# Kernel optimization log

Hardware: AMD Instinct MI355X
Metric: run time of the kernel (lower is better)

Reference implementation:

```python
import jax, jax.numpy as jnp
import numpy as np

H = 2048          # hidden_size
HK = 16           # linear_num_key_heads
HV = 32           # linear_num_value_heads
DK = 128          # linear_key_head_dim
DV = 128          # linear_value_head_dim
KW = 4            # linear_conv_kernel_dim
KEY_DIM = HK * DK   # 2048
VAL_DIM = HV * DV   # 4096
CONV_DIM = 2 * KEY_DIM + VAL_DIM  # 8192
T = 4096
EPS = 1e-6


def setup_inputs() -> dict:
    key = jax.random.key(0)
    ks = jax.random.split(key, 8)
    w = lambda k, shape, sc=0.02: (jax.random.normal(k, shape, jnp.float32) * sc)
    return {
        "hidden_states": jax.random.normal(ks[0], (T, H), jnp.float32),
        "W_qkvz": w(ks[1], (H, 2 * KEY_DIM + 2 * VAL_DIM)),   # q,k,v,z merged proj
        "W_ba": w(ks[2], (H, 2 * HV)),                        # b,a merged proj
        "conv_w": w(ks[3], (CONV_DIM, KW), 0.1),              # depthwise causal conv
        "A_log": jnp.log(jax.random.uniform(ks[4], (HV,), jnp.float32, 1.0, 16.0)),
        "dt_bias": jnp.ones((HV,), jnp.float32),
        "norm_w": jnp.ones((DV,), jnp.float32),
        "W_out": w(ks[5], (VAL_DIM, H)),
    }


def _l2norm(x):
    return x * jax.lax.rsqrt(jnp.sum(x * x, axis=-1, keepdims=True) + 1e-6)


def reference(hidden_states, W_qkvz, W_ba, conv_w, A_log, dt_bias, norm_w, W_out):
    T_ = hidden_states.shape[0]
    # 1. merged input projections
    qkvz = hidden_states @ W_qkvz                     # [T, 2*key+2*val]
    ba = hidden_states @ W_ba                         # [T, 2*HV]
    q, k, v, z = jnp.split(qkvz, [KEY_DIM, 2 * KEY_DIM, 2 * KEY_DIM + VAL_DIM], axis=-1)
    b, a = jnp.split(ba, 2, axis=-1)

    # 2. short causal depthwise conv1d over q|k|v (z is NOT convolved), then SiLU
    qkv = jnp.concatenate([q, k, v], axis=-1)         # [T, CONV_DIM]
    xp = jnp.pad(qkv, ((KW - 1, 0), (0, 0)))
    y = sum(xp[j:j + T_] * conv_w[:, j] for j in range(KW))
    qkv = jax.nn.silu(y)
    q, k, v = jnp.split(qkv, [KEY_DIM, 2 * KEY_DIM], axis=-1)

    q = _l2norm(q.reshape(T_, HK, DK)) * (DK ** -0.5)
    k = _l2norm(k.reshape(T_, HK, DK))
    v = v.reshape(T_, HV, DV)
    z = z.reshape(T_, HV, DV)

    # GQA-style head expansion
    r = HV // HK
    q = jnp.repeat(q, r, axis=1)                      # [T, HV, DK]
    k = jnp.repeat(k, r, axis=1)

    # gating / delta coefficients
    g = -jnp.exp(A_log) * jax.nn.softplus(a + dt_bias)  # [T, HV] log-decay
    beta = jax.nn.sigmoid(b)                            # [T, HV]

    # 3. gated delta rule recurrence: S_t = exp(g_t)*S + beta_t*k_t(v_t - k_t^T exp(g_t) S)
    def step(S, inp):
        q_t, k_t, v_t, g_t, b_t = inp
        S = S * jnp.exp(g_t)[:, None, None]             # [HV, DK, DV]
        kv = jnp.einsum('hd,hdv->hv', k_t, S)
        delta = (v_t - kv) * b_t[:, None]
        S = S + jnp.einsum('hd,hv->hdv', k_t, delta)
        o_t = jnp.einsum('hd,hdv->hv', q_t, S)
        return S, o_t

    S0 = jnp.zeros((HV, DK, DV), jnp.float32)
    _, o = jax.lax.scan(step, S0, (q, k, v, g, beta))   # o: [T, HV, DV]

    # 4. gated RMSNorm (norm_before_gate=True): rmsnorm(o)*w, then * silu(z)
    var = jnp.mean(o * o, axis=-1, keepdims=True)
    o = o * jax.lax.rsqrt(var + EPS) * norm_w
    o = o * jax.nn.silu(z)

    # 5. output projection
    return o.reshape(T_, VAL_DIM) @ W_out
```

## Files before the change

### kernel.cpp

```cpp
#include <hip/hip_runtime.h>
#include <hip/hip_bf16.h>

#define T_LEN 4096
#define H_DIM 2048
#define HKn 16
#define HVn 32
#define DKn 128
#define DVn 128
#define KEY_DIM 2048
#define VAL_DIM 4096

typedef unsigned int u32;
typedef unsigned short u16;
typedef __attribute__((ext_vector_type(8))) short bf16x8;
typedef __attribute__((ext_vector_type(4))) float f32x4;

__device__ __forceinline__ u16 f2bf(float x){
  u32 u = __float_as_uint(x);
  u32 r = (u + 0x7fffu + ((u>>16)&1u)) >> 16;
  return (u16)r;
}
__device__ __forceinline__ float bf2f(u32 b){ return __uint_as_float(b<<16); }
__device__ __forceinline__ u32 packbf(float a, float b){ return (u32)f2bf(a) | ((u32)f2bf(b)<<16); }

__global__ __launch_bounds__(256) void k_cvt(const float* __restrict__ in, u16* __restrict__ out, int n){
  int i = (blockIdx.x*256 + threadIdx.x)*8;
  if (i >= n) return;
  float4 a = *(const float4*)(in+i);
  float4 b = *(const float4*)(in+i+4);
  uint4 o;
  o.x = packbf(a.x,a.y); o.y = packbf(a.z,a.w);
  o.z = packbf(b.x,b.y); o.w = packbf(b.z,b.w);
  *(uint4*)(out+i) = o;
}

__global__ __launch_bounds__(256) void k_tcvt(const float* __restrict__ in, u16* __restrict__ out, int R, int C){
  __shared__ float tile[32][33];
  int c0 = blockIdx.x*32, r0 = blockIdx.y*32;
  int tx = threadIdx.x & 31, ty = threadIdx.x >> 5;
#pragma unroll
  for (int i=0;i<4;++i) tile[ty+8*i][tx] = in[(size_t)(r0+ty+8*i)*C + c0+tx];
  __syncthreads();
#pragma unroll
  for (int i=0;i<4;++i) out[(size_t)(c0+ty+8*i)*R + r0+tx] = f2bf(tile[tx][ty+8*i]);
}

__global__ __launch_bounds__(256) void k_ba(const float* __restrict__ X, const float* __restrict__ W,
    const float* __restrict__ A_log, const float* __restrict__ dt_bias,
    float* __restrict__ gT, float* __restrict__ bT){
  int tid = threadIdx.x;
  int t = blockIdx.x*4 + (tid>>6);
  int j = tid & 63;
  const float* xr = X + (size_t)t*H_DIM;
  float acc = 0.f;
  for (int k=0;k<H_DIM;k+=4){
    float4 xv = *(const float4*)(xr+k);
    acc += xv.x*W[(size_t)(k+0)*64 + j];
    acc += xv.y*W[(size_t)(k+1)*64 + j];
    acc += xv.z*W[(size_t)(k+2)*64 + j];
    acc += xv.w*W[(size_t)(k+3)*64 + j];
  }
  if (j < HVn) {
    bT[(size_t)j*T_LEN + t] = 1.f/(1.f+__expf(-acc));
  } else {
    int h = j - HVn;
    float x = acc + dt_bias[h];
    float sp = (x > 20.f) ? x : log1pf(__expf(x));
    gT[(size_t)h*T_LEN + t] = -__expf(A_log[h]) * sp;
  }
}

typedef const __attribute__((address_space(1))) u32* gas_t;
typedef __attribute__((address_space(3))) u32* las_t;
__device__ __forceinline__ void gld16(const void* g, void* l){
  __builtin_amdgcn_global_load_lds((gas_t)g, (las_t)l, 16, 0, 0);
}
__device__ __forceinline__ f32x4 mf(bf16x8 a, bf16x8 b, f32x4 c){
  return __builtin_amdgcn_mfma_f32_16x16x32_bf16(a,b,c,0,0,0);
}

#define G2_LDS 131072
#define SWX(a) ((a) ^ ((((a)>>9)&1)<<5))

template<int WRITE_BF16>
__global__ __launch_bounds__(512) void k_g256(const u16* __restrict__ A, const u16* __restrict__ BT,
    void* __restrict__ C1, void* __restrict__ C2, int NS, int M, int N, int K){
  extern __shared__ char sm[];
  const int tid=threadIdx.x, lane=tid&63, wave=tid>>6;
  const int fr=lane&15, fq=lane>>4;
  const int wm=wave>>2, wn=wave&3;
  const int nbm = M>>8, nwg = nbm*(N>>8);
  const int cpx = nwg>>3;
  const int swz = ((int)blockIdx.x & 7)*cpx + ((int)blockIdx.x >> 3);
  const int m0 = (swz % nbm) << 8, n0 = (swz / nbm) << 8;
  const int NK = K >> 5;

  f32x4 acc[8][4];
#pragma unroll
  for (int i=0;i<8;++i)
#pragma unroll
    for (int j=0;j<4;++j) acc[i][j] = (f32x4){0.f,0.f,0.f,0.f};

  auto stageA=[&](int kt){
    char* base = sm + (size_t)(kt&3)*32768;
#pragma unroll
    for (int ld=0; ld<2; ++ld){
      int p = ld*8192 + wave*1024 + lane*16;
      int a = SWX(p);
      gld16((const char*)A + ((size_t)(m0 + (a>>6))*K + kt*32)*2 + (a&63), base + p);
    }
  };
  auto stageB=[&](int kt){
    char* base = sm + (size_t)(kt&3)*32768 + 16384;
#pragma unroll
    for (int ld=0; ld<2; ++ld){
      int p = ld*8192 + wave*1024 + lane*16;
      int a = SWX(p);
      gld16((const char*)BT + ((size_t)(n0 + (a>>6))*K + kt*32)*2 + (a&63), base + p);
    }
  };

  stageA(0); stageB(0); stageA(1); stageB(1); stageA(2); stageB(2);
  __syncthreads();

  bf16x8 bcur[4], bnxt[4], a0f[4], a1f[4];
  {
    const char* bufA = sm;
    const char* bufB = sm + 16384;
#pragma unroll
    for (int j=0;j<4;++j){
      int a = (wn*64 + j*16 + fr)*64 + fq*16;
      bcur[j] = *(const bf16x8*)(bufB + SWX(a));
    }
#pragma unroll
    for (int i=0;i<4;++i){
      int a = (wm*128 + i*16 + fr)*64 + fq*16;
      a0f[i] = *(const bf16x8*)(bufA + SWX(a));
    }
  }

  for (int kt=0; kt<NK; ++kt){
    const char* bufA = sm + (size_t)(kt&3)*32768;
    if (kt+3 < NK) stageA(kt+3);
#pragma unroll
    for (int i=0;i<4;++i){
      int a = (wm*128 + 64 + i*16 + fr)*64 + fq*16;
      a1f[i] = *(const bf16x8*)(bufA + SWX(a));
    }
    asm volatile("s_waitcnt vmcnt(6)" ::: "memory");
    asm volatile("s_barrier" ::: "memory");
    __builtin_amdgcn_s_setprio(1);
#pragma unroll
    for (int i=0;i<4;++i)
#pragma unroll
      for (int j=0;j<4;++j) acc[i][j] = mf(a0f[i], bcur[j], acc[i][j]);
    __builtin_amdgcn_s_setprio(0);
    asm volatile("s_barrier" ::: "memory");
    if (kt+3 < NK) stageB(kt+3);
    if (kt+1 < NK){
      const char* nA = sm + (size_t)((kt+1)&3)*32768;
      const char* nB = nA + 16384;
#pragma unroll
      for (int j=0;j<4;++j){
        int a = (wn*64 + j*16 + fr)*64 + fq*16;
        bnxt[j] = *(const bf16x8*)(nB + SWX(a));
      }
#pragma unroll
      for (int i=0;i<4;++i){
        int a = (wm*128 + i*16 + fr)*64 + fq*16;
        a0f[i] = *(const bf16x8*)(nA + SWX(a));
      }
    }
    asm volatile("s_barrier" ::: "memory");
    __builtin_amdgcn_s_setprio(1);
#pragma unroll
    for (int i=0;i<4;++i)
#pragma unroll
      for (int j=0;j<4;++j) acc[4+i][j] = mf(a1f[i], bcur[j], acc[4+i][j]);
    __builtin_amdgcn_s_setprio(0);
    asm volatile("s_barrier" ::: "memory");
#pragma unroll
    for (int j=0;j<4;++j) bcur[j] = bnxt[j];
  }

#pragma unroll
  for (int mt=0; mt<8; ++mt)
#pragma unroll
    for (int nt=0; nt<4; ++nt){
      int row = m0 + wm*128 + mt*16 + fq*4;
      int col = n0 + wn*64 + nt*16 + fr;
#pragma unroll
      for (int r=0;r<4;++r){
        float v = acc[mt][nt][r];
        if (col < NS){
          if (WRITE_BF16) ((u16*)C1)[(size_t)(row+r)*NS + col] = f2bf(v);
          else            ((float*)C1)[(size_t)(row+r)*NS + col] = v;
        } else {
          if (WRITE_BF16) ((u16*)C2)[(size_t)(row+r)*(N-NS) + col-NS] = f2bf(v);
          else            ((float*)C2)[(size_t)(row+r)*(N-NS) + col-NS] = v;
        }
      }
    }
}

__global__ __launch_bounds__(256) void k_conv(const u16* __restrict__ qkv, const float* __restrict__ cw,
    u16* __restrict__ qn, u16* __restrict__ kn, u16* __restrict__ vv){
  int t = blockIdx.x;
  int region = blockIdx.y;
  int c = region*2048 + threadIdx.x*8;
  float wgt[8][4];
#pragma unroll
  for (int i=0;i<8;++i){
    float4 wv = *(const float4*)(cw + (size_t)(c+i)*4);
    wgt[i][0]=wv.x; wgt[i][1]=wv.y; wgt[i][2]=wv.z; wgt[i][3]=wv.w;
  }
  float y[8];
#pragma unroll
  for (int i=0;i<8;++i) y[i]=0.f;
#pragma unroll
  for (int j=0;j<4;++j){
    int tt = t + j - 3;
    if (tt < 0) continue;
    uint4 raw = *(const uint4*)(qkv + (size_t)tt*8192 + c);
    float xv[8];
    xv[0]=bf2f(raw.x&0xffffu); xv[1]=bf2f(raw.x>>16);
    xv[2]=bf2f(raw.y&0xffffu); xv[3]=bf2f(raw.y>>16);
    xv[4]=bf2f(raw.z&0xffffu); xv[5]=bf2f(raw.z>>16);
    xv[6]=bf2f(raw.w&0xffffu); xv[7]=bf2f(raw.w>>16);
#pragma unroll
    for (int i=0;i<8;++i) y[i] += xv[i]*wgt[i][j];
  }
#pragma unroll
  for (int i=0;i<8;++i){ y[i] = y[i] / (1.f + __expf(-y[i])); }

  if (region <= 1){
    float ss = 0.f;
#pragma unroll
    for (int i=0;i<8;++i) ss += y[i]*y[i];
    ss += __shfl_xor(ss,1); ss += __shfl_xor(ss,2);
    ss += __shfl_xor(ss,4); ss += __shfl_xor(ss,8);
    float sc = 1.f/sqrtf(ss + 1e-6f);
    if (region==0) sc *= 0.08838834764831845f;
#pragma unroll
    for (int i=0;i<8;++i) y[i]*=sc;
    u16* dst = (region==0 ? qn : kn) + (size_t)t*KEY_DIM + (c - region*2048);
    *(uint4*)dst = make_uint4(packbf(y[0],y[1]),packbf(y[2],y[3]),packbf(y[4],y[5]),packbf(y[6],y[7]));
  } else {
    u16* dst = vv + (size_t)t*VAL_DIM + (c - 4096);
    *(uint4*)dst = make_uint4(packbf(y[0],y[1]),packbf(y[2],y[3]),packbf(y[4],y[5]),packbf(y[6],y[7]));
  }
}

#define P1_K    0
#define P1_Q    16384
#define P1_KT   32768
#define P1_NBP  49152
#define P1_AQ   57344
#define P1_DT   65536
#define P1_WMT  73728
#define P1_NBD  81920
#define P1_TII  86016
#define P1_R1T  90112
#define P1_TAB  94208
#define P1_SIZE 95296

#define SW7(r,cb) ((cb) ^ (((r)&7)<<4))
#define SW3(r,cb) ((cb) ^ (((r)&3)<<4))
#define aK(r,cb)   (P1_K   + (r)*256 + SW7(r,cb))
#define aQ2(r,cb)  (P1_Q   + (r)*256 + SW7(r,cb))
#define aKT(d,cb)  (P1_KT  + (d)*128 + SW7(d,cb))
#define aNBP(t,cb) (P1_NBP + (t)*128 + SW7(t,cb))
#define aAQ(t,cb)  (P1_AQ  + (t)*128 + SW7(t,cb))
#define aDT(s,cb)  (P1_DT  + (s)*128 + SW7(s,cb))
#define aWMT(s,cb) (P1_WMT + (s)*128 + SW7(s,cb))
#define aTII(b,r,cb) (P1_TII + (b)*1024 + (r)*64 + SW3(r,cb))
#define aR1T(v,cb)   (P1_R1T + (v)*64 + SW3(v,cb))

__global__ __launch_bounds__(256) void k_prep(const u16* __restrict__ qn, const u16* __restrict__ kn,
    const float* __restrict__ gT, const float* __restrict__ bT,
    u16* __restrict__ aqmg, u16* __restrict__ kwmg, float* __restrict__ tabg){
  extern __shared__ char sm[];
  const int tid=threadIdx.x, lane=tid&63, wave=tid>>6;
  const int fr=lane&15, fq=lane>>4;
  const int b=blockIdx.x, h=b>>6, c=b&63, kh=h>>1;
  const f32x4 z4={0.f,0.f,0.f,0.f};
  for (int off=P1_DT+tid*16; off<P1_TAB; off+=4096) *(uint4*)(sm+off)=make_uint4(0,0,0,0);
  {
    int srow = wave*4 + (lane>>4);
    int pb = (lane&15)*16;
#pragma unroll
    for (int r=0;r<4;++r){
      int row=r*16+srow;
      int gcb = pb ^ ((row&7)<<4);
      gld16((const char*)kn + ((size_t)((c<<6)+row)*KEY_DIM + kh*DKn)*2 + gcb, sm + P1_K + r*4096 + wave*1024);
      gld16((const char*)qn + ((size_t)((c<<6)+row)*KEY_DIM + kh*DKn)*2 + gcb, sm + P1_Q + r*4096 + wave*1024);
    }
  }
  float* TB=(float*)(sm+P1_TAB);
  if (wave==0){
    int t=lane;
    float gv=gT[(size_t)h*T_LEN+(c<<6)+t];
    float bv=bT[(size_t)h*T_LEN+(c<<6)+t];
    float s=gv;
    for(int o2=1;o2<64;o2<<=1){ float u=__shfl_up(s,o2,64); if(lane>=o2) s+=u; }
    float cgL=__shfl(s,63,64);
    float gam=__expf(s);
    TB[t]=s; TB[64+t]=gam; TB[128+t]=__expf(cgL-s); TB[192+t]=bv;
    float* tg=tabg+(size_t)b*192;
    tg[t]=gam; tg[64+t]=bv;
    if(t==0) tg[128]=__expf(cgL);
  }
  __syncthreads();
#pragma unroll
  for (int dd=0;dd<2;++dd){
    int tp=tid&31, d0=((tid>>5)+dd*8)*8;
    bf16x8 r0=*(const bf16x8*)(sm+aK(2*tp,d0*2));
    bf16x8 r1=*(const bf16x8*)(sm+aK(2*tp+1,d0*2));
#pragma unroll
    for(int j=0;j<8;++j){
      u32 pk=((u32)(u16)r0[j])|((u32)(u16)r1[j]<<16);
      *(u32*)(sm+aKT(d0+j,tp*4))=pk;
    }
  }
  const int ra=(wave>>1)*32, rb=(wave&1)*32;
  f32x4 kq[2][2], qk[2][2];
#pragma unroll
  for(int ta=0;ta<2;++ta)
#pragma unroll
  for(int tb=0;tb<2;++tb){ kq[ta][tb]=z4; qk[ta][tb]=z4; }
#pragma unroll
  for(int kk=0;kk<4;++kk){
    int cb=kk*64+fq*16;
    bf16x8 Ak0=*(const bf16x8*)(sm+aK(ra+fr,cb));
    bf16x8 Ak1=*(const bf16x8*)(sm+aK(ra+16+fr,cb));
    bf16x8 Aq0=*(const bf16x8*)(sm+aQ2(ra+fr,cb));
    bf16x8 Aq1=*(const bf16x8*)(sm+aQ2(ra+16+fr,cb));
    bf16x8 Bk0=*(const bf16x8*)(sm+aK(rb+fr,cb));
    bf16x8 Bk1=*(const bf16x8*)(sm+aK(rb+16+fr,cb));
    if(ra>=rb)      { kq[0][0]=mf(Ak0,Bk0,kq[0][0]); qk[0][0]=mf(Aq0,Bk0,qk[0][0]); }
    if(ra>=rb+16)   { kq[0][1]=mf(Ak0,Bk1,kq[0][1]); qk[0][1]=mf(Aq0,Bk1,qk[0][1]); }
    if(ra+16>=rb)   { kq[1][0]=mf(Ak1,Bk0,kq[1][0]); qk[1][0]=mf(Aq1,Bk0,qk[1][0]); }
    if(ra+16>=rb+16){ kq[1][1]=mf(Ak1,Bk1,kq[1][1]); qk[1][1]=mf(Aq1,Bk1,qk[1][1]); }
  }
  {
    const float* cg=TB; const float* Be=TB+192;
#pragma unroll
    for(int ta=0;ta<2;++ta)
#pragma unroll
    for(int tb=0;tb<2;++tb){
      int tab=ra+16*ta, tbb=rb+16*tb;
#pragma unroll
      for(int p=0;p<4;++p){
        int t=tab+fq*4+p, s2=tbb+fr;
        float e=__expf(cg[t]-cg[s2]);
        float nv=(s2<t)? -Be[t]*kq[ta][tb][p]*e : 0.f;
        *(u16*)(sm+aNBP(t,s2*2)) = (tbb<tab)? f2bf(nv):(u16)0;
        if(tbb==tab) ((float*)(sm+P1_NBD))[(tab>>4)*256+(fq*4+p)*16+fr]=nv;
        float av=(s2<=t)? qk[ta][tb][p]*e : 0.f;
        *(u16*)(sm+aAQ(t,s2*2)) = f2bf(av);
      }
    }
  }
  __syncthreads();
  {
    int r=lane&15;
    const float* nb=(const float*)(sm+P1_NBD)+wave*256+r*16;
    float n[16], t_[16];
#pragma unroll
    for(int j=0;j<16;++j){ n[j]=nb[j]; t_[j]=(j==r)?1.f:0.f; }
#pragma unroll
    for(int s=0;s<15;++s){
      float tsj[16];
#pragma unroll
      for(int j=0;j<16;++j)
        tsj[j]=__int_as_float(__builtin_amdgcn_ds_bpermute(s*4,__float_as_int(t_[j])));
      if(r>s){
#pragma unroll
        for(int j=0;j<16;++j) t_[j]=fmaf(n[s],tsj[j],t_[j]);
      }
    }
    if(lane<16){
      u32 pk[8];
#pragma unroll
      for(int j=0;j<8;++j) pk[j]=packbf(t_[2*j],t_[2*j+1]);
      *(uint4*)(sm+aTII(wave,r,0)) =make_uint4(pk[0],pk[1],pk[2],pk[3]);
      *(uint4*)(sm+aTII(wave,r,16))=make_uint4(pk[4],pk[5],pk[6],pk[7]);
    }
  }
  __syncthreads();
  {
    const float* WV=TB+128;
    int vb=16*wave;
    for(int i=0;i<4;++i){
      f32x4 acc;
#pragma unroll
      for(int p=0;p<4;++p) acc[p]=(vb+fr==16*i+fq*4+p)?1.f:0.f;
      int np=(i+1)>>1;
      for(int jp=0;jp<np;++jp){
        bf16x8 A=*(const bf16x8*)(sm+aNBP(16*i+fr,jp*64+fq*16));
        bf16x8 B=*(const bf16x8*)(sm+aDT(vb+fr,jp*64+fq*16));
        acc=mf(A,B,acc);
      }
      uint2 w1; w1.x=packbf(acc[0],acc[1]); w1.y=packbf(acc[2],acc[3]);
      *(uint2*)(sm+aR1T(vb+fr,fq*8))=w1;
      bf16x8 At=*(const bf16x8*)(sm+aTII(i,fr,fq*16));
      bf16x8 Bt=*(const bf16x8*)(sm+aR1T(vb+fr,fq*16));
      f32x4 dl=mf(At,Bt,z4);
      int s0=16*i+fq*4;
      uint2 wd; wd.x=packbf(dl[0],dl[1]); wd.y=packbf(dl[2],dl[3]);
      *(uint2*)(sm+aDT(vb+fr,s0*2))=wd;
      uint2 ww; ww.x=packbf(dl[0]*WV[s0],dl[1]*WV[s0+1]); ww.y=packbf(dl[2]*WV[s0+2],dl[3]*WV[s0+3]);
      *(uint2*)(sm+aWMT(vb+fr,s0*2))=ww;
    }
  }
  __syncthreads();
  {
    u16* aout = aqmg + (size_t)b*4096;
#pragma unroll
    for(int ts=0;ts<4;++ts){
      f32x4 acc=z4;
#pragma unroll
      for(int jp=0;jp<2;++jp){
        bf16x8 A=*(const bf16x8*)(sm+aAQ(16*wave+fr,jp*64+fq*16));
        bf16x8 B=*(const bf16x8*)(sm+aDT(16*ts+fr,jp*64+fq*16));
        acc=mf(A,B,acc);
      }
#pragma unroll
      for(int p=0;p<4;++p){
        int t=16*wave+fq*4+p, s=16*ts+fr;
        aout[(t*128 + ((s*2)^((t&7)<<4)))>>1]=f2bf(acc[p]);
      }
    }
    u16* kout = kwmg + (size_t)b*8192;
#pragma unroll
    for(int j=0;j<2;++j){
      int dt=wave+4*j;
#pragma unroll
      for(int st=0;st<4;++st){
        f32x4 acc=z4;
#pragma unroll
        for(int jp=0;jp<2;++jp){
          bf16x8 A=*(const bf16x8*)(sm+aKT(16*dt+fr,jp*64+fq*16));
          bf16x8 B=*(const bf16x8*)(sm+aWMT(16*st+fr,jp*64+fq*16));
          acc=mf(A,B,acc);
        }
#pragma unroll
        for(int p=0;p<4;++p){
          int d=16*dt+fq*4+p, s=16*st+fr;
          kout[(d*128 + ((s*2)^((d&7)<<4)))>>1]=f2bf(acc[p]);
        }
      }
    }
  }
}

#define P2_K(b)   ((b)*16384)
#define P2_Q(b)   (32768 + (b)*16384)
#define P2_W(b)   (65536 + (b)*16384)
#define P2_M(b)   (98304 + (b)*8192)
#define P2_TAB(b) (114688 + (b)*1024)
#define P2_ST(b)  (116736 + (b)*4096)
#define P2_R0T    124928
#define P2_SIZE   126976

#define bKx(b,r,cb)  (P2_K(b) + (r)*256 + SW7(r,cb))
#define bQx(b,r,cb)  (P2_Q(b) + (r)*256 + SW7(r,cb))
#define bWx(b,d,cb)  (P2_W(b) + (d)*128 + SW7(d,cb))
#define bMx(b,t,cb)  (P2_M(b) + (t)*128 + SW7(t,cb))
#define bSTx(b,v,cb) (P2_ST(b) + (v)*256 + SW7(v,cb))
#define bRx(v,cb)    (P2_R0T + (v)*128 + SW7(v,cb))

__global__ __launch_bounds__(256) void k_state(const u16* __restrict__ qn, const u16* __restrict__ kn,
    const u16* __restrict__ vv, const u16* __restrict__ aqmg, const u16* __restrict__ kwmg,
    const float* __restrict__ tabg, float* __restrict__ o){
  extern __shared__ char sm[];
  const int tid=threadIdx.x, lane=tid&63, wave=tid>>6;
  const int fr=lane&15, fq=lane>>4;
  const int h=blockIdx.x&31, vs=(blockIdx.x>>5)*16, kh=h>>1;
  const f32x4 z4={0.f,0.f,0.f,0.f};
  for(int off=116736+tid*16; off<124928; off+=4096) *(uint4*)(sm+off)=make_uint4(0,0,0,0);

  auto stage=[&](int c,int b){
    int srow=wave*4+(lane>>4);
    int pb2=(lane&15)*16;
#pragma unroll
    for(int r=0;r<4;++r){
      int row=r*16+srow;
      int gcb=pb2^((row&7)<<4);
      gld16((const char*)kn + ((size_t)((c<<6)+row)*KEY_DIM + kh*DKn)*2 + gcb, sm + P2_K(b)+r*4096+wave*1024);
      gld16((const char*)qn + ((size_t)((c<<6)+row)*KEY_DIM + kh*DKn)*2 + gcb, sm + P2_Q(b)+r*4096+wave*1024);
    }
    const char* wsrc=(const char*)kwmg + (size_t)(h*64+c)*16384;
#pragma unroll
    for(int r=0;r<4;++r)
      gld16(wsrc + r*4096 + wave*1024 + lane*16, sm + P2_W(b)+r*4096+wave*1024);
    const char* msrc=(const char*)aqmg + (size_t)(h*64+c)*8192;
#pragma unroll
    for(int r=0;r<2;++r)
      gld16(msrc + r*4096 + wave*1024 + lane*16, sm + P2_M(b)+r*4096+wave*1024);
    if(wave==0)
      gld16((const char*)tabg + (size_t)(h*64+c)*768 + lane*16, sm + P2_TAB(b));
  };
  u16 vl[4];
  auto loadV=[&](int c){
#pragma unroll
    for(int p=0;p<4;++p)
      vl[p]=vv[(size_t)((c<<6)+16*wave+fq*4+p)*VAL_DIM + h*DVn + vs + fr];
  };

  f32x4 S0=z4, S1=z4;
  stage(0,0); loadV(0);
  __syncthreads();

  for(int c=0;c<64;++c){
    int b=c&1;
    const float* TBf=(const float*)(sm+P2_TAB(b));
    f32x4 ks=z4;
#pragma unroll
    for(int kk=0;kk<4;++kk)
      ks=mf(*(const bf16x8*)(sm+bKx(b,16*wave+fr,kk*64+fq*16)),
            *(const bf16x8*)(sm+bSTx(b,fr,kk*64+fq*16)), ks);
    float r0v[4];
#pragma unroll
    for(int p=0;p<4;++p){
      int t=16*wave+fq*4+p;
      r0v[p]=TBf[64+t]*(bf2f(vl[p]) - TBf[t]*ks[p]);
    }
    uint2 rw; rw.x=packbf(r0v[0],r0v[1]); rw.y=packbf(r0v[2],r0v[3]);
    *(uint2*)(sm+bRx(fr,32*wave+8*fq))=rw;
    __syncthreads();
    if(c<63) stage(c+1,b^1);
    f32x4 qs=z4;
#pragma unroll
    for(int kk=0;kk<4;++kk)
      qs=mf(*(const bf16x8*)(sm+bQx(b,16*wave+fr,kk*64+fq*16)),
            *(const bf16x8*)(sm+bSTx(b,fr,kk*64+fq*16)), qs);
#pragma unroll
    for(int p=0;p<4;++p) qs[p]*=TBf[16*wave+fq*4+p];
#pragma unroll
    for(int jp=0;jp<2;++jp)
      qs=mf(*(const bf16x8*)(sm+bMx(b,16*wave+fr,jp*64+fq*16)),
            *(const bf16x8*)(sm+bRx(fr,jp*64+fq*16)), qs);
#pragma unroll
    for(int p=0;p<4;++p)
      o[(size_t)((c<<6)+16*wave+fq*4+p)*VAL_DIM + h*DVn + vs + fr]=qs[p];
    if(c<63) loadV(c+1);
    float gl=TBf[128];
    S0[0]*=gl;S0[1]*=gl;S0[2]*=gl;S0[3]*=gl;
    S1[0]*=gl;S1[1]*=gl;S1[2]*=gl;S1[3]*=gl;
#pragma unroll
    for(int jp=0;jp<2;++jp){
      bf16x8 Br=*(const bf16x8*)(sm+bRx(fr,jp*64+fq*16));
      S0=mf(*(const bf16x8*)(sm+bWx(b,16*wave+fr,jp*64+fq*16)), Br, S0);
      S1=mf(*(const bf16x8*)(sm+bWx(b,16*(wave+4)+fr,jp*64+fq*16)), Br, S1);
    }
    uint2 s0w; s0w.x=packbf(S0[0],S0[1]); s0w.y=packbf(S0[2],S0[3]);
    *(uint2*)(sm+bSTx(b^1,fr,32*wave+8*fq))=s0w;
    uint2 s1w; s1w.x=packbf(S1[0],S1[1]); s1w.y=packbf(S1[2],S1[3]);
    *(uint2*)(sm+bSTx(b^1,fr,32*(wave+4)+8*fq))=s1w;
    __syncthreads();
  }
}

__global__ __launch_bounds__(256) void k_gnorm(const float* __restrict__ o, const u16* __restrict__ zq,
    const float* __restrict__ nw, u16* __restrict__ og){
  int t = blockIdx.x;
  int base = threadIdx.x*16;
  const float* src = o + (size_t)t*VAL_DIM + base;
  float x[16];
#pragma unroll
  for (int i=0;i<4;++i){
    float4 f = *(const float4*)(src + i*4);
    x[i*4+0]=f.x; x[i*4+1]=f.y; x[i*4+2]=f.z; x[i*4+3]=f.w;
  }
  float ss=0.f;
#pragma unroll
  for (int i=0;i<16;++i) ss += x[i]*x[i];
  ss += __shfl_xor(ss,1); ss += __shfl_xor(ss,2); ss += __shfl_xor(ss,4);
  float rs = 1.f/sqrtf(ss*(1.f/128.f) + 1e-6f);
  const u16* zp = zq + (size_t)t*VAL_DIM + base;
  uint4 z0 = *(const uint4*)zp;
  uint4 z1 = *(const uint4*)(zp+8);
  u32 zr[8] = {z0.x,z0.y,z0.z,z0.w,z1.x,z1.y,z1.z,z1.w};
  u32 outw[8];
#pragma unroll
  for (int p=0;p<8;++p){
    float za = bf2f(zr[p]&0xffffu), zb = bf2f(zr[p]>>16);
    float sa = za/(1.f+__expf(-za)), sb = zb/(1.f+__expf(-zb));
    int i0 = p*2, i1 = p*2+1;
    float oa = x[i0]*rs*nw[(base+i0)&127]*sa;
    float ob = x[i1]*rs*nw[(base+i1)&127]*sb;
    outw[p] = packbf(oa, ob);
  }
  uint4* dst = (uint4*)(og + (size_t)t*VAL_DIM + base);
  dst[0] = make_uint4(outw[0],outw[1],outw[2],outw[3]);
  dst[1] = make_uint4(outw[4],outw[5],outw[6],outw[7]);
}

extern "C" void kernel_launch(void* const* d_in, const int* in_sizes, int n_in,
                              void* d_out, int out_size, void* d_ws, size_t ws_size,
                              hipStream_t stream) {
  const float* hidden  = (const float*)d_in[0];
  const float* W_qkvz  = (const float*)d_in[1];
  const float* W_ba    = (const float*)d_in[2];
  const float* conv_w  = (const float*)d_in[3];
  const float* A_log   = (const float*)d_in[4];
  const float* dt_bias = (const float*)d_in[5];
  const float* norm_w  = (const float*)d_in[6];
  const float* W_out   = (const float*)d_in[7];

  char* w = (char*)d_ws;
  size_t need = 252706816;
  if (ws_size < need) return;

  u16*   Xb   = (u16*)(w + 0);
  u16*   W1T  = (u16*)(w + 16777216);
  u16*   QKV  = (u16*)(w + 67108864);
  u16*   Z    = (u16*)(w + 134217728);
  u16*   QN   = (u16*)(w + 167772160);
  u16*   KN   = (u16*)(w + 184549376);
  u16*   V    = (u16*)(w + 201326592);
  u16*   WoT  = (u16*)(w + 234881024);
  float* GTb  = (float*)(w + 251658240);
  float* BTb  = (float*)(w + 252182528);
  float* O    = (float*)(w + 0);
  u16*   AQMg = (u16*)(w + 67108864);
  u16*   KWMg = (u16*)(w + 83886080);
  float* TABg = (float*)(w + 117440512);
  u16*   OG   = (u16*)(w + 167772160);

  static int smem_set = 0;
  if (!smem_set){
    hipFuncSetAttribute((const void*)k_prep,  hipFuncAttributeMaxDynamicSharedMemorySize, P1_SIZE);
    hipFuncSetAttribute((const void*)k_state, hipFuncAttributeMaxDynamicSharedMemorySize, P2_SIZE);
    hipFuncSetAttribute((const void*)k_g256<1>, hipFuncAttributeMaxDynamicSharedMemorySize, G2_LDS);
    hipFuncSetAttribute((const void*)k_g256<0>, hipFuncAttributeMaxDynamicSharedMemorySize, G2_LDS);
    smem_set = 1;
  }

  k_cvt<<<4096,256,0,stream>>>(hidden, Xb, T_LEN*H_DIM);
  k_tcvt<<<dim3(12288/32, H_DIM/32),256,0,stream>>>(W_qkvz, W1T, H_DIM, 12288);
  k_tcvt<<<dim3(H_DIM/32, VAL_DIM/32),256,0,stream>>>(W_out, WoT, VAL_DIM, H_DIM);
  k_ba<<<T_LEN/4,256,0,stream>>>(hidden, W_ba, A_log, dt_bias, GTb, BTb);
  k_g256<1><<<768,512,G2_LDS,stream>>>(Xb, W1T, QKV, Z, 8192, T_LEN, 12288, H_DIM);
  k_conv<<<dim3(T_LEN,4),256,0,stream>>>(QKV, conv_w, QN, KN, V);
  k_prep<<<2048,256,P1_SIZE,stream>>>(QN, KN, GTb, BTb, AQMg, KWMg, TABg);
  k_state<<<256,256,P2_SIZE,stream>>>(QN, KN, V, AQMg, KWMg, TABg, O);
  k_gnorm<<<T_LEN,256,0,stream>>>(O, Z, norm_w, OG);
  k_g256<0><<<128,512,G2_LDS,stream>>>(OG, WoT, d_out, d_out, H_DIM, T_LEN, H_DIM, VAL_DIM);
}
```

Measured before the change: 818.0 us.

## Restructure GEMM pipeline, add smaller-tile output GEMM, sliding-window conv, bf16 state output

The main GEMM loop now loads A and B fragments from LDS inside each k-step and drops cross-iteration register prefetching, with a different vmcnt wait point. A new 128x256-tile GEMM kernel replaces the 256-tile one for the output projection so it launches 256 blocks instead of 128 and fills more CUs. The conv kernel processes 32 timesteps per block with a register sliding window, so each input row is read about once instead of four times. The recurrence output is stored as bf16 instead of fp32 to halve that traffic, at some cost in precision.

```diff
diff --git a/kernel.cpp b/kernel.cpp
--- a/kernel.cpp
+++ b/kernel.cpp
@@ -123,64 +123,44 @@
   stageA(0); stageB(0); stageA(1); stageB(1); stageA(2); stageB(2);
   __syncthreads();
 
-  bf16x8 bcur[4], bnxt[4], a0f[4], a1f[4];
-  {
-    const char* bufA = sm;
-    const char* bufB = sm + 16384;
+  for (int kt=0; kt<NK; ++kt){
+    const char* bufA = sm + (size_t)(kt&3)*32768;
+    const char* bufB = bufA + 16384;
+    bf16x8 bfr[4], afr[4];
 #pragma unroll
     for (int j=0;j<4;++j){
       int a = (wn*64 + j*16 + fr)*64 + fq*16;
-      bcur[j] = *(const bf16x8*)(bufB + SWX(a));
+      bfr[j] = *(const bf16x8*)(bufB + SWX(a));
     }
 #pragma unroll
     for (int i=0;i<4;++i){
       int a = (wm*128 + i*16 + fr)*64 + fq*16;
-      a0f[i] = *(const bf16x8*)(bufA + SWX(a));
-    }
-  }
-
-  for (int kt=0; kt<NK; ++kt){
-    const char* bufA = sm + (size_t)(kt&3)*32768;
+      afr[i] = *(const bf16x8*)(bufA + SWX(a));
+    }
     if (kt+3 < NK) stageA(kt+3);
+    asm volatile("s_barrier" ::: "memory");
+    __builtin_amdgcn_s_setprio(1);
+#pragma unroll
+    for (int i=0;i<4;++i)
+#pragma unroll
+      for (int j=0;j<4;++j) acc[i][j] = mf(afr[i], bfr[j], acc[i][j]);
+    __builtin_amdgcn_s_setprio(0);
+    asm volatile("s_barrier" ::: "memory");
 #pragma unroll
     for (int i=0;i<4;++i){
       int a = (wm*128 + 64 + i*16 + fr)*64 + fq*16;
-      a1f[i] = *(const bf16x8*)(bufA + SWX(a));
-    }
-    asm volatile("s_waitcnt vmcnt(6)" ::: "memory");
+      afr[i] = *(const bf16x8*)(bufA + SWX(a));
+    }
+    if (kt+3 < NK) stageB(kt+3);
     asm volatile("s_barrier" ::: "memory");
     __builtin_amdgcn_s_setprio(1);
 #pragma unroll
     for (int i=0;i<4;++i)
 #pragma unroll
-      for (int j=0;j<4;++j) acc[i][j] = mf(a0f[i], bcur[j], acc[i][j]);
+      for (int j=0;j<4;++j) acc[4+i][j] = mf(afr[i], bfr[j], acc[4+i][j]);
     __builtin_amdgcn_s_setprio(0);
+    asm volatile("s_waitcnt vmcnt(8)" ::: "memory");
     asm volatile("s_barrier" ::: "memory");
-    if (kt+3 < NK) stageB(kt+3);
-    if (kt+1 < NK){
-      const char* nA = sm + (size_t)((kt+1)&3)*32768;
-      const char* nB = nA + 16384;
-#pragma unroll
-      for (int j=0;j<4;++j){
-        int a = (wn*64 + j*16 + fr)*64 + fq*16;
-        bnxt[j] = *(const bf16x8*)(nB + SWX(a));
-      }
-#pragma unroll
-      for (int i=0;i<4;++i){
-        int a = (wm*128 + i*16 + fr)*64 + fq*16;
-        a0f[i] = *(const bf16x8*)(nA + SWX(a));
-      }
-    }
-    asm volatile("s_barrier" ::: "memory");
-    __builtin_amdgcn_s_setprio(1);
-#pragma unroll
-    for (int i=0;i<4;++i)
-#pragma unroll
-      for (int j=0;j<4;++j) acc[4+i][j] = mf(a1f[i], bcur[j], acc[4+i][j]);
-    __builtin_amdgcn_s_setprio(0);
-    asm volatile("s_barrier" ::: "memory");
-#pragma unroll
-    for (int j=0;j<4;++j) bcur[j] = bnxt[j];
   }
 
 #pragma unroll
@@ -203,51 +183,128 @@
     }
 }
 
+#define GW_LDS 98304
+__global__ __launch_bounds__(512) void k_gw(const u16* __restrict__ A, const u16* __restrict__ BT,
+    float* __restrict__ C, int M, int N, int K){
+  extern __shared__ char sm[];
+  const int tid=threadIdx.x, lane=tid&63, wave=tid>>6;
+  const int fr=lane&15, fq=lane>>4;
+  const int wm=wave>>2, wn=wave&3;
+  const int nbm=M>>7, nwg=nbm*(N>>8);
+  const int cpx=nwg>>3;
+  const int swz=((int)blockIdx.x&7)*cpx + ((int)blockIdx.x>>3);
+  const int m0=(swz%nbm)<<7, n0=(swz/nbm)<<8;
+  const int NK=K>>5;
+
+  f32x4 acc[4][4];
+#pragma unroll
+  for(int i=0;i<4;++i)
+#pragma unroll
+    for(int j=0;j<4;++j) acc[i][j]=(f32x4){0.f,0.f,0.f,0.f};
+
+  auto stage=[&](int kt){
+    char* base = sm + (size_t)(kt&3)*24576;
+    { int p=tid*16; int a=SWX(p);
+      gld16((const char*)A + ((size_t)(m0+(a>>6))*K + kt*32)*2 + (a&63), base+p); }
+    char* bb = base + 8192;
+#pragma unroll
+    for(int ld=0;ld<2;++ld){ int p=ld*8192+tid*16; int a=SWX(p);
+      gld16((const char*)BT + ((size_t)(n0+(a>>6))*K + kt*32)*2 + (a&63), bb+p); }
+  };
+  stage(0); stage(1); stage(2);
+  __syncthreads();
+
+  for(int kt=0;kt<NK;++kt){
+    const char* bufA = sm + (size_t)(kt&3)*24576;
+    const char* bufB = bufA + 8192;
+    bf16x8 afr[4], bfr[4];
+#pragma unroll
+    for(int i=0;i<4;++i){ int a=(wm*64+i*16+fr)*64+fq*16; afr[i]=*(const bf16x8*)(bufA+SWX(a)); }
+#pragma unroll
+    for(int j=0;j<4;++j){ int a=(wn*64+j*16+fr)*64+fq*16; bfr[j]=*(const bf16x8*)(bufB+SWX(a)); }
+    if(kt+3<NK) stage(kt+3);
+    asm volatile("s_barrier":::"memory");
+    __builtin_amdgcn_s_setprio(1);
+#pragma unroll
+    for(int i=0;i<4;++i)
+#pragma unroll
+      for(int j=0;j<4;++j) acc[i][j]=mf(afr[i],bfr[j],acc[i][j]);
+    __builtin_amdgcn_s_setprio(0);
+    asm volatile("s_waitcnt vmcnt(6)":::"memory");
+    asm volatile("s_barrier":::"memory");
+  }
+
+#pragma unroll
+  for(int mt=0;mt<4;++mt)
+#pragma unroll
+    for(int nt=0;nt<4;++nt){
+      int row=m0+wm*64+mt*16+fq*4;
+      int col=n0+wn*64+nt*16+fr;
+#pragma unroll
+      for(int r=0;r<4;++r)
+        C[(size_t)(row+r)*N + col] = acc[mt][nt][r];
+    }
+}
+
 __global__ __launch_bounds__(256) void k_conv(const u16* __restrict__ qkv, const float* __restrict__ cw,
     u16* __restrict__ qn, u16* __restrict__ kn, u16* __restrict__ vv){
-  int t = blockIdx.x;
-  int region = blockIdx.y;
-  int c = region*2048 + threadIdx.x*8;
+  const int r = blockIdx.y;
+  const int t0 = blockIdx.x*32;
+  const int c = r*2048 + threadIdx.x*8;
   float wgt[8][4];
 #pragma unroll
-  for (int i=0;i<8;++i){
-    float4 wv = *(const float4*)(cw + (size_t)(c+i)*4);
-    wgt[i][0]=wv.x; wgt[i][1]=wv.y; wgt[i][2]=wv.z; wgt[i][3]=wv.w;
-  }
-  float y[8];
-#pragma unroll
-  for (int i=0;i<8;++i) y[i]=0.f;
-#pragma unroll
-  for (int j=0;j<4;++j){
-    int tt = t + j - 3;
-    if (tt < 0) continue;
-    uint4 raw = *(const uint4*)(qkv + (size_t)tt*8192 + c);
-    float xv[8];
-    xv[0]=bf2f(raw.x&0xffffu); xv[1]=bf2f(raw.x>>16);
-    xv[2]=bf2f(raw.y&0xffffu); xv[3]=bf2f(raw.y>>16);
-    xv[4]=bf2f(raw.z&0xffffu); xv[5]=bf2f(raw.z>>16);
-    xv[6]=bf2f(raw.w&0xffffu); xv[7]=bf2f(raw.w>>16);
-#pragma unroll
-    for (int i=0;i<8;++i) y[i] += xv[i]*wgt[i][j];
-  }
-#pragma unroll
-  for (int i=0;i<8;++i){ y[i] = y[i] / (1.f + __expf(-y[i])); }
-
-  if (region <= 1){
-    float ss = 0.f;
-#pragma unroll
-    for (int i=0;i<8;++i) ss += y[i]*y[i];
-    ss += __shfl_xor(ss,1); ss += __shfl_xor(ss,2);
-    ss += __shfl_xor(ss,4); ss += __shfl_xor(ss,8);
-    float sc = 1.f/sqrtf(ss + 1e-6f);
-    if (region==0) sc *= 0.08838834764831845f;
-#pragma unroll
-    for (int i=0;i<8;++i) y[i]*=sc;
-    u16* dst = (region==0 ? qn : kn) + (size_t)t*KEY_DIM + (c - region*2048);
-    *(uint4*)dst = make_uint4(packbf(y[0],y[1]),packbf(y[2],y[3]),packbf(y[4],y[5]),packbf(y[6],y[7]));
+  for(int i=0;i<8;++i){
+    float4 wv=*(const float4*)(cw+(size_t)(c+i)*4);
+    wgt[i][0]=wv.x;wgt[i][1]=wv.y;wgt[i][2]=wv.z;wgt[i][3]=wv.w;
+  }
+  float h0[8],h1[8],h2[8];
+  if(t0>=3){
+    uint4 a=*(const uint4*)(qkv+(size_t)(t0-3)*8192+c);
+    uint4 b=*(const uint4*)(qkv+(size_t)(t0-2)*8192+c);
+    uint4 d=*(const uint4*)(qkv+(size_t)(t0-1)*8192+c);
+    h0[0]=bf2f(a.x&0xffffu);h0[1]=bf2f(a.x>>16);h0[2]=bf2f(a.y&0xffffu);h0[3]=bf2f(a.y>>16);
+    h0[4]=bf2f(a.z&0xffffu);h0[5]=bf2f(a.z>>16);h0[6]=bf2f(a.w&0xffffu);h0[7]=bf2f(a.w>>16);
+    h1[0]=bf2f(b.x&0xffffu);h1[1]=bf2f(b.x>>16);h1[2]=bf2f(b.y&0xffffu);h1[3]=bf2f(b.y>>16);
+    h1[4]=bf2f(b.z&0xffffu);h1[5]=bf2f(b.z>>16);h1[6]=bf2f(b.w&0xffffu);h1[7]=bf2f(b.w>>16);
+    h2[0]=bf2f(d.x&0xffffu);h2[1]=bf2f(d.x>>16);h2[2]=bf2f(d.y&0xffffu);h2[3]=bf2f(d.y>>16);
+    h2[4]=bf2f(d.z&0xffffu);h2[5]=bf2f(d.z>>16);h2[6]=bf2f(d.w&0xffffu);h2[7]=bf2f(d.w>>16);
   } else {
-    u16* dst = vv + (size_t)t*VAL_DIM + (c - 4096);
-    *(uint4*)dst = make_uint4(packbf(y[0],y[1]),packbf(y[2],y[3]),packbf(y[4],y[5]),packbf(y[6],y[7]));
+#pragma unroll
+    for(int i=0;i<8;++i){h0[i]=0.f;h1[i]=0.f;h2[i]=0.f;}
+  }
+  uint4 c0=*(const uint4*)(qkv+(size_t)t0*8192+c);
+  uint4 c1=*(const uint4*)(qkv+(size_t)(t0+1)*8192+c);
+  uint4 c2=*(const uint4*)(qkv+(size_t)(t0+2)*8192+c);
+  for(int it=0; it<32; ++it){
+    int t=t0+it;
+    uint4 cn = (t+3<T_LEN)? *(const uint4*)(qkv+(size_t)(t+3)*8192+c) : c0;
+    float cur[8];
+    cur[0]=bf2f(c0.x&0xffffu);cur[1]=bf2f(c0.x>>16);cur[2]=bf2f(c0.y&0xffffu);cur[3]=bf2f(c0.y>>16);
+    cur[4]=bf2f(c0.z&0xffffu);cur[5]=bf2f(c0.z>>16);cur[6]=bf2f(c0.w&0xffffu);cur[7]=bf2f(c0.w>>16);
+    float y[8];
+#pragma unroll
+    for(int i=0;i<8;++i)
+      y[i]=fmaf(h0[i],wgt[i][0],fmaf(h1[i],wgt[i][1],fmaf(h2[i],wgt[i][2],cur[i]*wgt[i][3])));
+#pragma unroll
+    for(int i=0;i<8;++i) y[i]=y[i]/(1.f+__expf(-y[i]));
+    if(r<=1){
+      float ss=0.f;
+#pragma unroll
+      for(int i=0;i<8;++i) ss+=y[i]*y[i];
+      ss+=__shfl_xor(ss,1);ss+=__shfl_xor(ss,2);ss+=__shfl_xor(ss,4);ss+=__shfl_xor(ss,8);
+      float sc=1.f/sqrtf(ss+1e-6f);
+      if(r==0) sc*=0.08838834764831845f;
+#pragma unroll
+      for(int i=0;i<8;++i) y[i]*=sc;
+      u16* dst=(r==0?qn:kn)+(size_t)t*KEY_DIM+(c-r*2048);
+      *(uint4*)dst=make_uint4(packbf(y[0],y[1]),packbf(y[2],y[3]),packbf(y[4],y[5]),packbf(y[6],y[7]));
+    } else {
+      u16* dst=vv+(size_t)t*VAL_DIM+(c-4096);
+      *(uint4*)dst=make_uint4(packbf(y[0],y[1]),packbf(y[2],y[3]),packbf(y[4],y[5]),packbf(y[6],y[7]));
+    }
+#pragma unroll
+    for(int i=0;i<8;++i){h0[i]=h1[i];h1[i]=h2[i];h2[i]=cur[i];}
+    c0=c1;c1=c2;c2=cn;
   }
 }
 
@@ -472,7 +529,7 @@
 
 __global__ __launch_bounds__(256) void k_state(const u16* __restrict__ qn, const u16* __restrict__ kn,
     const u16* __restrict__ vv, const u16* __restrict__ aqmg, const u16* __restrict__ kwmg,
-    const float* __restrict__ tabg, float* __restrict__ o){
+    const float* __restrict__ tabg, u16* __restrict__ ob){
   extern __shared__ char sm[];
   const int tid=threadIdx.x, lane=tid&63, wave=tid>>6;
   const int fr=lane&15, fq=lane>>4;
@@ -543,7 +600,7 @@
             *(const bf16x8*)(sm+bRx(fr,jp*64+fq*16)), qs);
 #pragma unroll
     for(int p=0;p<4;++p)
-      o[(size_t)((c<<6)+16*wave+fq*4+p)*VAL_DIM + h*DVn + vs + fr]=qs[p];
+      ob[(size_t)((c<<6)+16*wave+fq*4+p)*VAL_DIM + h*DVn + vs + fr]=f2bf(qs[p]);
     if(c<63) loadV(c+1);
     float gl=TBf[128];
     S0[0]*=gl;S0[1]*=gl;S0[2]*=gl;S0[3]*=gl;
@@ -562,17 +619,17 @@
   }
 }
 
-__global__ __launch_bounds__(256) void k_gnorm(const float* __restrict__ o, const u16* __restrict__ zq,
+__global__ __launch_bounds__(256) void k_gnorm(const u16* __restrict__ ob, const u16* __restrict__ zq,
     const float* __restrict__ nw, u16* __restrict__ og){
   int t = blockIdx.x;
   int base = threadIdx.x*16;
-  const float* src = o + (size_t)t*VAL_DIM + base;
+  const u16* src = ob + (size_t)t*VAL_DIM + base;
+  uint4 a0 = *(const uint4*)src;
+  uint4 a1 = *(const uint4*)(src+8);
+  u32 xr[8] = {a0.x,a0.y,a0.z,a0.w,a1.x,a1.y,a1.z,a1.w};
   float x[16];
 #pragma unroll
-  for (int i=0;i<4;++i){
-    float4 f = *(const float4*)(src + i*4);
-    x[i*4+0]=f.x; x[i*4+1]=f.y; x[i*4+2]=f.z; x[i*4+3]=f.w;
-  }
+  for (int p=0;p<8;++p){ x[2*p]=bf2f(xr[p]&0xffffu); x[2*p+1]=bf2f(xr[p]>>16); }
   float ss=0.f;
 #pragma unroll
   for (int i=0;i<16;++i) ss += x[i]*x[i];
@@ -589,8 +646,8 @@
     float sa = za/(1.f+__expf(-za)), sb = zb/(1.f+__expf(-zb));
     int i0 = p*2, i1 = p*2+1;
     float oa = x[i0]*rs*nw[(base+i0)&127]*sa;
-    float ob = x[i1]*rs*nw[(base+i1)&127]*sb;
-    outw[p] = packbf(oa, ob);
+    float obv = x[i1]*rs*nw[(base+i1)&127]*sb;
+    outw[p] = packbf(oa, obv);
   }
   uint4* dst = (uint4*)(og + (size_t)t*VAL_DIM + base);
   dst[0] = make_uint4(outw[0],outw[1],outw[2],outw[3]);
@@ -623,7 +680,7 @@
   u16*   WoT  = (u16*)(w + 234881024);
   float* GTb  = (float*)(w + 251658240);
   float* BTb  = (float*)(w + 252182528);
-  float* O    = (float*)(w + 0);
+  u16*   OB   = (u16*)(w + 0);
   u16*   AQMg = (u16*)(w + 67108864);
   u16*   KWMg = (u16*)(w + 83886080);
   float* TABg = (float*)(w + 117440512);
@@ -634,7 +691,7 @@
     hipFuncSetAttribute((const void*)k_prep,  hipFuncAttributeMaxDynamicSharedMemorySize, P1_SIZE);
     hipFuncSetAttribute((const void*)k_state, hipFuncAttributeMaxDynamicSharedMemorySize, P2_SIZE);
     hipFuncSetAttribute((const void*)k_g256<1>, hipFuncAttributeMaxDynamicSharedMemorySize, G2_LDS);
-    hipFuncSetAttribute((const void*)k_g256<0>, hipFuncAttributeMaxDynamicSharedMemorySize, G2_LDS);
+    hipFuncSetAttribute((const void*)k_gw, hipFuncAttributeMaxDynamicSharedMemorySize, GW_LDS);
     smem_set = 1;
   }
 
@@ -643,9 +700,9 @@
   k_tcvt<<<dim3(H_DIM/32, VAL_DIM/32),256,0,stream>>>(W_out, WoT, VAL_DIM, H_DIM);
   k_ba<<<T_LEN/4,256,0,stream>>>(hidden, W_ba, A_log, dt_bias, GTb, BTb);
   k_g256<1><<<768,512,G2_LDS,stream>>>(Xb, W1T, QKV, Z, 8192, T_LEN, 12288, H_DIM);
-  k_conv<<<dim3(T_LEN,4),256,0,stream>>>(QKV, conv_w, QN, KN, V);
+  k_conv<<<dim3(128,4),256,0,stream>>>(QKV, conv_w, QN, KN, V);
   k_prep<<<2048,256,P1_SIZE,stream>>>(QN, KN, GTb, BTb, AQMg, KWMg, TABg);
-  k_state<<<256,256,P2_SIZE,stream>>>(QN, KN, V, AQMg, KWMg, TABg, O);
-  k_gnorm<<<T_LEN,256,0,stream>>>(O, Z, norm_w, OG);
-  k_g256<0><<<128,512,G2_LDS,stream>>>(OG, WoT, d_out, d_out, H_DIM, T_LEN, H_DIM, VAL_DIM);
-}
+  k_state<<<256,256,P2_SIZE,stream>>>(QN, KN, V, AQMg, KWMg, TABg, OB);
+  k_gnorm<<<T_LEN,256,0,stream>>>(OB, Z, norm_w, OG);
+  k_gw<<<256,512,GW_LDS,stream>>>(OG, WoT, (float*)d_out, T_LEN, H_DIM, VAL_DIM);
+}
```

Result: faster. 697.2 us (-14.8%).
